# Optimization experiments

Hardware: AMD Instinct MI355X
Metric: run time of the kernel (lower is better)

## Reference

```python
import jax, jax.numpy as jnp
import numpy as np

DIM = 512
NUM_HEADS = 8
HEAD_SIZE = 64
INNER = NUM_HEADS * HEAD_SIZE  # 512


def setup_inputs() -> dict:
    key = jax.random.key(0)
    k1, k2, k3, k4, k5 = jax.random.split(key, 5)
    x = jax.random.normal(k1, (2, 4096, DIM), dtype=jnp.float32)
    # Linear params stored as [in, out] for y = x @ W + b (same math as torch Linear)
    w_qkv = jax.random.normal(k2, (DIM, INNER * 3), dtype=jnp.float32) * (1.0 / np.sqrt(DIM))
    b_qkv = jax.random.normal(k3, (INNER * 3,), dtype=jnp.float32) * 0.01
    w_out = jax.random.normal(k4, (INNER, DIM), dtype=jnp.float32) * (1.0 / np.sqrt(INNER))
    b_out = jax.random.normal(k5, (DIM,), dtype=jnp.float32) * 0.01
    return {"x": x, "w_qkv": w_qkv, "b_qkv": b_qkv, "w_out": w_out, "b_out": b_out}


def reference(x, w_qkv, b_qkv, w_out, b_out):
    b, n, _ = x.shape
    qkv = x @ w_qkv + b_qkv                      # [b, n, 3*inner]
    q, k, v = jnp.split(qkv, 3, axis=-1)          # each [b, n, inner]

    def heads(t):  # 'b n (h d) -> b h n d'
        return t.reshape(b, n, NUM_HEADS, HEAD_SIZE).transpose(0, 2, 1, 3)

    q, k, v = heads(q), heads(k), heads(v)
    scores = jnp.einsum('bhnd,bhmd->bhnm', q, k) / jnp.sqrt(jnp.float32(HEAD_SIZE))
    probs = jax.nn.softmax(scores, axis=-1)       # dropout is identity in eval
    out = jnp.einsum('bhnm,bhmd->bhnd', probs, v)
    out = out.transpose(0, 2, 1, 3).reshape(b, n, INNER)  # 'b h n d -> b n (h d)'
    return out @ w_out + b_out
```

## Files before the change

### kernel.cpp

```cpp
#include <hip/hip_runtime.h>

typedef __bf16 bf16;
typedef __bf16 bf16x8 __attribute__((ext_vector_type(8)));
typedef float f32x4 __attribute__((ext_vector_type(4)));
typedef unsigned u32x4 __attribute__((ext_vector_type(4)));
typedef unsigned u32;

#define MFMA16(a, b, c) __builtin_amdgcn_mfma_f32_16x16x32_bf16((a), (b), (c), 0, 0, 0)

static __device__ __forceinline__ bf16x8 ldg8(const bf16* p) {
  return *(const bf16x8*)p;
}
static __device__ __forceinline__ unsigned cvt_pk_bf16(float lo, float hi) {
  unsigned d;
  asm("v_cvt_pk_bf16_f32 %0, %1, %2" : "=v"(d) : "v"(lo), "v"(hi));
  return d;
}
static __device__ __forceinline__ void pl32_swap(unsigned& a, unsigned& b) {
  asm("v_permlane32_swap_b32 %0, %1" : "+v"(a), "+v"(b));
}
static __device__ __forceinline__ void pl16_swap(unsigned& a, unsigned& b) {
  asm("v_permlane16_swap_b32 %0, %1" : "+v"(a), "+v"(b));
}
static __device__ __forceinline__ void async_lds16(const bf16* g, bf16* l) {
  __builtin_amdgcn_global_load_lds(
      (const __attribute__((address_space(1))) u32*)(const void*)g,
      (__attribute__((address_space(3))) u32*)(void*)l, 16, 0, 0);
}


__global__ __launch_bounds__(256) void cvt_pack_x(const float* __restrict__ x,
                                                  bf16* __restrict__ Xp) {
  int mt = blockIdx.x, kc = blockIdx.y;
  int r = threadIdx.x >> 1;
  int khalf = threadIdx.x & 1;
  const float* src = x + (size_t)(mt * 128 + r) * 512 + kc * 32 + khalf * 16;
  float4 v0 = *(const float4*)(src + 0);
  float4 v1 = *(const float4*)(src + 4);
  float4 v2 = *(const float4*)(src + 8);
  float4 v3 = *(const float4*)(src + 12);
  bf16* tile = Xp + ((size_t)mt * 16 + kc) * 4096;
  bf16x8 a, b;
  a[0] = (bf16)v0.x; a[1] = (bf16)v0.y; a[2] = (bf16)v0.z; a[3] = (bf16)v0.w;
  a[4] = (bf16)v1.x; a[5] = (bf16)v1.y; a[6] = (bf16)v1.z; a[7] = (bf16)v1.w;
  b[0] = (bf16)v2.x; b[1] = (bf16)v2.y; b[2] = (bf16)v2.z; b[3] = (bf16)v2.w;
  b[4] = (bf16)v3.x; b[5] = (bf16)v3.y; b[6] = (bf16)v3.z; b[7] = (bf16)v3.w;
  int kc0 = khalf * 2;
  *(bf16x8*)&tile[(kc0 + 0) * 1024 + r * 8] = a;
  *(bf16x8*)&tile[(kc0 + 1) * 1024 + r * 8] = b;
}

__global__ __launch_bounds__(256) void transpose_pack_w(const float* __restrict__ W,
                                                        bf16* __restrict__ Wp,
                                                        int N) {
  __shared__ float tile[32 * 129];
  int kc = blockIdx.x, nt = blockIdx.y;
  int row = threadIdx.x >> 3;
  int c0 = (threadIdx.x & 7) * 16;
  const float* src = W + (size_t)(kc * 32 + row) * N + nt * 128 + c0;
#pragma unroll
  for (int i = 0; i < 4; i++) {
    float4 v = *(const float4*)(src + i * 4);
    tile[row * 129 + c0 + i * 4 + 0] = v.x;
    tile[row * 129 + c0 + i * 4 + 1] = v.y;
    tile[row * 129 + c0 + i * 4 + 2] = v.z;
    tile[row * 129 + c0 + i * 4 + 3] = v.w;
  }
  __syncthreads();
  bf16* dst = Wp + ((size_t)nt * 16 + kc) * 4096;
#pragma unroll
  for (int half = 0; half < 2; half++) {
    int U = threadIdx.x + half * 256;
    int kchunk = U >> 7, n = U & 127;
    bf16x8 o;
#pragma unroll
    for (int j = 0; j < 8; j++) o[j] = (bf16)tile[(kchunk * 8 + j) * 129 + n];
    *(bf16x8*)&dst[U * 8] = o;
  }
}

static __device__ __forceinline__ void stage_tile(const bf16* __restrict__ g,
                                                  bf16* l, int wave, int lane) {
#pragma unroll
  for (int c = 0; c < 2; c++) {
    int chunk = wave * 2 + c;
    async_lds16(g + chunk * 512 + lane * 8, l + chunk * 512);
  }
}

__device__ __forceinline__ void gemm128_core(const bf16* __restrict__ At,
                                             const bf16* __restrict__ Bt,
                                             bf16* Ab0, bf16* Ab1, bf16* Bb0,
                                             bf16* Bb1, int wave, int lane,
                                             int wr, int wc, int l16, int quad,
                                             f32x4 acc[4][4]) {
  stage_tile(At, Ab0, wave, lane);
  stage_tile(Bt, Bb0, wave, lane);
  __syncthreads();
#pragma unroll 2
  for (int kc = 0; kc < 16; kc++) {
    bf16* Ab = (kc & 1) ? Ab1 : Ab0;
    bf16* Bb = (kc & 1) ? Bb1 : Bb0;
    if (kc < 15) {
      bf16* An = (kc & 1) ? Ab0 : Ab1;
      bf16* Bn = (kc & 1) ? Bb0 : Bb1;
      stage_tile(At + (kc + 1) * 4096, An, wave, lane);
      stage_tile(Bt + (kc + 1) * 4096, Bn, wave, lane);
    }
    bf16x8 af[4], bf[4];
#pragma unroll
    for (int fi = 0; fi < 4; fi++)
      af[fi] = *(const bf16x8*)&Ab[(quad * 128 + wr * 64 + fi * 16 + l16) * 8];
#pragma unroll
    for (int fj = 0; fj < 4; fj++)
      bf[fj] = *(const bf16x8*)&Bb[(quad * 128 + wc * 64 + fj * 16 + l16) * 8];
    __builtin_amdgcn_s_setprio(1);
#pragma unroll
    for (int fi = 0; fi < 4; fi++)
#pragma unroll
      for (int fj = 0; fj < 4; fj++)
        acc[fi][fj] = MFMA16(af[fi], bf[fj], acc[fi][fj]);
    __builtin_amdgcn_s_setprio(0);
    __syncthreads();
  }
}

__global__ __launch_bounds__(256, 3) void qkv_gemm(const bf16* __restrict__ Xp,
                                                   const bf16* __restrict__ Wp1,
                                                   const float* __restrict__ bqkv,
                                                   bf16* __restrict__ Q,
                                                   bf16* __restrict__ Kh,
                                                   bf16* __restrict__ Vt) {
  int mt = blockIdx.x, nt = blockIdx.y;
  int tid = threadIdx.x;
  int wave = tid >> 6, lane = tid & 63;
  int l16 = lane & 15, quad = lane >> 4;
  int wr = wave >> 1, wc = wave & 1;

  __shared__ __align__(16) bf16 Ab[2][4096];
  __shared__ __align__(16) bf16 Bb[2][4096];

  f32x4 acc[4][4] = {};
  gemm128_core(Xp + (size_t)mt * 16 * 4096, Wp1 + (size_t)nt * 16 * 4096,
               Ab[0], Ab[1], Bb[0], Bb[1], wave, lane, wr, wc, l16, quad, acc);

#pragma unroll
  for (int fj = 0; fj < 4; fj++) {
    int c = nt * 128 + wc * 64 + fj * 16 + l16;
    float bias = bqkv[c];
    int which = c >> 9, inner = c & 511;
    int h = inner >> 6, d = inner & 63;
#pragma unroll
    for (int fi = 0; fi < 4; fi++) {
#pragma unroll
      for (int r = 0; r < 4; r++) {
        int m = mt * 128 + wr * 64 + fi * 16 + quad * 4 + r;
        int b = m >> 12, n = m & 4095;
        int bh = b * 8 + h;
        float v = acc[fi][fj][r] + bias;
        if (which == 0)
          Q[((size_t)bh * 4096 + n) * 64 + d] = (bf16)(v * 0.18033688f);
        else if (which == 1)
          Kh[((size_t)bh * 4096 + n) * 64 + d] = (bf16)v;
        else
          Vt[(((size_t)bh * 64 + (n >> 6)) * 64 + d) * 64 + (n & 63)] = (bf16)v;
      }
    }
  }
}

__global__ __launch_bounds__(256, 4) void flash_partial(const bf16* __restrict__ Q,
                                                        const bf16* __restrict__ K,
                                                        const bf16* __restrict__ Vt,
                                                        bf16* __restrict__ Opart,
                                                        float* __restrict__ Lpart) {
  int strip = blockIdx.x, bh = blockIdx.y, qtr = blockIdx.z;
  int tid = threadIdx.x;
  int wave = tid >> 6, lane = tid & 63;
  int l16 = lane & 15, quad = lane >> 4;

  const bf16* Qh = Q + (size_t)bh * 4096 * 64;
  const bf16* Kg = K + ((size_t)bh * 4096 + qtr * 1024) * 64;
  const bf16* Vg = Vt + (size_t)bh * 64 * 4096 + (size_t)qtr * 1024 * 64;

  __shared__ __align__(16) bf16 Klds[2][4096];
  __shared__ __align__(16) bf16 Vlds[2][4096];

  int qbase = strip * 128 + wave * 32;
  bf16x8 aq[2][2];
#pragma unroll
  for (int mt = 0; mt < 2; mt++) {
    const bf16* qr = Qh + (size_t)(qbase + mt * 16 + l16) * 64;
    aq[mt][0] = ldg8(qr + quad * 8);
    aq[mt][1] = ldg8(qr + 32 + quad * 8);
  }

  bf16x8 ones;
#pragma unroll
  for (int i = 0; i < 8; i++) ones[i] = (bf16)1.0f;

  f32x4 o[2][4] = {};
  f32x4 acc_l[2] = {};

  int e0 = tid * 8, e1 = (256 + tid) * 8;
  int r0 = e0 >> 6, r1 = e1 >> 6;
  int u0 = r0 * 8 + (((e0 & 63) >> 3) ^ (r0 & 7));
  int u1 = r1 * 8 + (((e1 & 63) >> 3) ^ (r1 & 7));

  bf16x8 kp0 = ldg8(Kg + e0), kp1 = ldg8(Kg + e1);
  bf16x8 vp0 = ldg8(Vg + e0), vp1 = ldg8(Vg + e1);

#pragma unroll 2
  for (int t = 0; t < 16; t++) {
    int cur = t & 1;
    bf16* kl = Klds[cur];
    bf16* vl = Vlds[cur];
    *(bf16x8*)&kl[u0 * 8] = kp0;
    *(bf16x8*)&kl[u1 * 8] = kp1;
    *(bf16x8*)&vl[u0 * 8] = vp0;
    *(bf16x8*)&vl[u1 * 8] = vp1;
    __syncthreads();

    if (t < 15) {
      const bf16* kg = Kg + (size_t)(t + 1) * 4096;
      const bf16* vg = Vg + (size_t)(t + 1) * 4096;
      kp0 = ldg8(kg + e0);
      kp1 = ldg8(kg + e1);
      vp0 = ldg8(vg + e0);
      vp1 = ldg8(vg + e1);
    }

#pragma unroll
    for (int h2 = 0; h2 < 2; h2++) {
      f32x4 s[2][2] = {};
      __builtin_amdgcn_s_setprio(1);
#pragma unroll
      for (int c2 = 0; c2 < 2; c2++) {
        int n = h2 * 32 + c2 * 16 + l16;
        bf16x8 k0 = *(const bf16x8*)&kl[(n * 8 + (quad ^ (n & 7))) * 8];
        bf16x8 k1 = *(const bf16x8*)&kl[(n * 8 + ((4 + quad) ^ (n & 7))) * 8];
#pragma unroll
        for (int mt = 0; mt < 2; mt++) {
          s[mt][c2] = MFMA16(k0, aq[mt][0], s[mt][c2]);
          s[mt][c2] = MFMA16(k1, aq[mt][1], s[mt][c2]);
        }
      }
      __builtin_amdgcn_s_setprio(0);

      bf16x8 pa[2];
#pragma unroll
      for (int mt = 0; mt < 2; mt++) {
        unsigned ue[2], wo[2];
#pragma unroll
        for (int c2 = 0; c2 < 2; c2++) {
          float p0 = __builtin_amdgcn_exp2f(s[mt][c2][0]);
          float p1 = __builtin_amdgcn_exp2f(s[mt][c2][1]);
          float p2 = __builtin_amdgcn_exp2f(s[mt][c2][2]);
          float p3 = __builtin_amdgcn_exp2f(s[mt][c2][3]);
          ue[c2] = cvt_pk_bf16(p0, p1);
          wo[c2] = cvt_pk_bf16(p2, p3);
        }
        pl32_swap(ue[0], ue[1]);
        pl16_swap(ue[0], ue[1]);
        pl32_swap(wo[0], wo[1]);
        pl16_swap(wo[0], wo[1]);
        u32x4 pk = {ue[0], wo[0], ue[1], wo[1]};
        pa[mt] = __builtin_bit_cast(bf16x8, pk);
      }

      __builtin_amdgcn_s_setprio(1);
      acc_l[0] = MFMA16(pa[0], ones, acc_l[0]);
      acc_l[1] = MFMA16(pa[1], ones, acc_l[1]);
#pragma unroll
      for (int ct = 0; ct < 4; ct++) {
        int d = ct * 16 + l16;
        bf16x8 bv = *(const bf16x8*)&vl[(d * 8 + ((h2 * 4 + quad) ^ (d & 7))) * 8];
        o[0][ct] = MFMA16(pa[0], bv, o[0][ct]);
        o[1][ct] = MFMA16(pa[1], bv, o[1][ct]);
      }
      __builtin_amdgcn_s_setprio(0);
    }
  }

  size_t ub = ((size_t)qtr * 16 + bh) * 32 + strip;
  bf16* op = Opart + ub * 8192;
#pragma unroll
  for (int mt = 0; mt < 2; mt++) {
#pragma unroll
    for (int ct = 0; ct < 4; ct++)
#pragma unroll
      for (int r = 0; r < 4; r++)
        op[(wave * 32 + mt * 16 + quad * 4 + r) * 64 + ct * 16 + l16] =
            (bf16)o[mt][ct][r];
    if (l16 == 0) {
#pragma unroll
      for (int r = 0; r < 4; r++)
        Lpart[ub * 128 + wave * 32 + mt * 16 + quad * 4 + r] = acc_l[mt][r];
    }
  }
}

__global__ __launch_bounds__(256) void flash_combine(const bf16* __restrict__ Opart,
                                                     const float* __restrict__ Lpart,
                                                     bf16* __restrict__ Ap) {
  int mt = blockIdx.x, kc = blockIdx.y;
  int b = mt >> 5, strip = mt & 31;
  int h = kc >> 1, d0 = (kc & 1) * 32;
  int bh = b * 8 + h;
  size_t u[4];
#pragma unroll
  for (int q = 0; q < 4; q++) u[q] = ((size_t)q * 16 + bh) * 32 + strip;
  bf16* dst = Ap + ((size_t)mt * 16 + kc) * 4096;
#pragma unroll
  for (int hf = 0; hf < 2; hf++) {
    int U = threadIdx.x + hf * 256;
    int kchunk = U >> 7, r = U & 127;
    float acc[8] = {};
    float ls = 0.f;
#pragma unroll
    for (int q = 0; q < 4; q++) {
      bf16x8 ov = ldg8(&Opart[u[q] * 8192 + r * 64 + d0 + kchunk * 8]);
#pragma unroll
      for (int j = 0; j < 8; j++) acc[j] += (float)ov[j];
      ls += Lpart[u[q] * 128 + r];
    }
    float rl = 1.0f / ls;
    bf16x8 o;
#pragma unroll
    for (int j = 0; j < 8; j++) o[j] = (bf16)(acc[j] * rl);
    *(bf16x8*)&dst[U * 8] = o;
  }
}

__global__ __launch_bounds__(256, 3) void out_gemm(const bf16* __restrict__ Ap,
                                                   const bf16* __restrict__ Wp2,
                                                   const float* __restrict__ bout,
                                                   float* __restrict__ Out) {
  int mt = blockIdx.x, nt = blockIdx.y;
  int tid = threadIdx.x;
  int wave = tid >> 6, lane = tid & 63;
  int l16 = lane & 15, quad = lane >> 4;
  int wr = wave >> 1, wc = wave & 1;

  __shared__ __align__(16) bf16 Ab[2][4096];
  __shared__ __align__(16) bf16 Bb[2][4096];

  f32x4 acc[4][4] = {};
  gemm128_core(Ap + (size_t)mt * 16 * 4096, Wp2 + (size_t)nt * 16 * 4096,
               Ab[0], Ab[1], Bb[0], Bb[1], wave, lane, wr, wc, l16, quad, acc);

#pragma unroll
  for (int fj = 0; fj < 4; fj++) {
    int c = nt * 128 + wc * 64 + fj * 16 + l16;
    float bias = bout[c];
#pragma unroll
    for (int fi = 0; fi < 4; fi++) {
#pragma unroll
      for (int r = 0; r < 4; r++) {
        int m = mt * 128 + wr * 64 + fi * 16 + quad * 4 + r;
        Out[(size_t)m * 512 + c] = acc[fi][fj][r] + bias;
      }
    }
  }
}

extern "C" void kernel_launch(void* const* d_in, const int* in_sizes, int n_in,
                              void* d_out, int out_size, void* d_ws,
                              size_t ws_size, hipStream_t stream) {
  const float* x = (const float*)d_in[0];
  const float* w_qkv = (const float*)d_in[1];
  const float* b_qkv = (const float*)d_in[2];
  const float* w_out = (const float*)d_in[3];
  const float* b_out = (const float*)d_in[4];
  float* out = (float*)d_out;

  char* ws = (char*)d_ws;
  bf16* Q = (bf16*)(ws + 0);
  bf16* K = (bf16*)(ws + 8388608);
  bf16* Vt = (bf16*)(ws + 16777216);
  bf16* Wp2 = (bf16*)(ws + 25165824);
  bf16* Opart = (bf16*)(ws + 25690112);
  float* Lpart = (float*)(ws + 59244544);
  bf16* Xp = (bf16*)(ws + 25690112);
  bf16* Wp1 = (bf16*)(ws + 34078720);
  bf16* Ap = (bf16*)(ws + 0);

  cvt_pack_x<<<dim3(64, 16), 256, 0, stream>>>(x, Xp);
  transpose_pack_w<<<dim3(16, 12), 256, 0, stream>>>(w_qkv, Wp1, 1536);
  transpose_pack_w<<<dim3(16, 4), 256, 0, stream>>>(w_out, Wp2, 512);
  qkv_gemm<<<dim3(64, 12), 256, 0, stream>>>(Xp, Wp1, b_qkv, Q, K, Vt);
  flash_partial<<<dim3(32, 16, 4), 256, 0, stream>>>(Q, K, Vt, Opart, Lpart);
  flash_combine<<<dim3(64, 16), 256, 0, stream>>>(Opart, Lpart, Ap);
  out_gemm<<<dim3(64, 4), 256, 0, stream>>>(Ap, Wp2, b_out, out);
}
```

Measured before the change: 208.2 us.

## Fuse x fp32-to-bf16 conversion into QKV GEMM and stage epilogue through LDS

Removes the separate cvt_pack_x kernel by having qkv_gemm load fp32 x directly, convert to bf16 in registers and write it into LDS. The two weight-pack launches are merged into one. The QKV epilogue now goes through an LDS tile so that Q, K and V^T are written with coalesced 16-byte stores instead of scattered 2-byte stores. Both GEMMs replace async global-to-LDS loads with register prefetch plus LDS stores. Each GEMM tile now re-reads fp32 x, twice the bytes of bf16, and the register-staged loads may hide latency less well than the async path.

```diff
diff --git a/kernel.cpp b/kernel.cpp
--- a/kernel.cpp
+++ b/kernel.cpp
@@ -4,7 +4,6 @@
 typedef __bf16 bf16x8 __attribute__((ext_vector_type(8)));
 typedef float f32x4 __attribute__((ext_vector_type(4)));
 typedef unsigned u32x4 __attribute__((ext_vector_type(4)));
-typedef unsigned u32;
 
 #define MFMA16(a, b, c) __builtin_amdgcn_mfma_f32_16x16x32_bf16((a), (b), (c), 0, 0, 0)
 
@@ -22,42 +21,27 @@
 static __device__ __forceinline__ void pl16_swap(unsigned& a, unsigned& b) {
   asm("v_permlane16_swap_b32 %0, %1" : "+v"(a), "+v"(b));
 }
-static __device__ __forceinline__ void async_lds16(const bf16* g, bf16* l) {
-  __builtin_amdgcn_global_load_lds(
-      (const __attribute__((address_space(1))) u32*)(const void*)g,
-      (__attribute__((address_space(3))) u32*)(void*)l, 16, 0, 0);
-}
-
-
-__global__ __launch_bounds__(256) void cvt_pack_x(const float* __restrict__ x,
-                                                  bf16* __restrict__ Xp) {
-  int mt = blockIdx.x, kc = blockIdx.y;
-  int r = threadIdx.x >> 1;
-  int khalf = threadIdx.x & 1;
-  const float* src = x + (size_t)(mt * 128 + r) * 512 + kc * 32 + khalf * 16;
-  float4 v0 = *(const float4*)(src + 0);
-  float4 v1 = *(const float4*)(src + 4);
-  float4 v2 = *(const float4*)(src + 8);
-  float4 v3 = *(const float4*)(src + 12);
-  bf16* tile = Xp + ((size_t)mt * 16 + kc) * 4096;
-  bf16x8 a, b;
-  a[0] = (bf16)v0.x; a[1] = (bf16)v0.y; a[2] = (bf16)v0.z; a[3] = (bf16)v0.w;
-  a[4] = (bf16)v1.x; a[5] = (bf16)v1.y; a[6] = (bf16)v1.z; a[7] = (bf16)v1.w;
-  b[0] = (bf16)v2.x; b[1] = (bf16)v2.y; b[2] = (bf16)v2.z; b[3] = (bf16)v2.w;
-  b[4] = (bf16)v3.x; b[5] = (bf16)v3.y; b[6] = (bf16)v3.z; b[7] = (bf16)v3.w;
-  int kc0 = khalf * 2;
-  *(bf16x8*)&tile[(kc0 + 0) * 1024 + r * 8] = a;
-  *(bf16x8*)&tile[(kc0 + 1) * 1024 + r * 8] = b;
-}
-
-__global__ __launch_bounds__(256) void transpose_pack_w(const float* __restrict__ W,
-                                                        bf16* __restrict__ Wp,
-                                                        int N) {
+
+
+__global__ __launch_bounds__(256) void pack_weights(const float* __restrict__ Wqkv,
+                                                    const float* __restrict__ Wout,
+                                                    bf16* __restrict__ Wp1,
+                                                    bf16* __restrict__ Wp2) {
   __shared__ float tile[32 * 129];
   int kc = blockIdx.x, nt = blockIdx.y;
+  const float* W;
+  bf16* dst;
+  int N, ntl;
+  if (nt < 12) {
+    W = Wqkv; N = 1536; ntl = nt;
+    dst = Wp1 + ((size_t)ntl * 16 + kc) * 4096;
+  } else {
+    W = Wout; N = 512; ntl = nt - 12;
+    dst = Wp2 + ((size_t)ntl * 16 + kc) * 4096;
+  }
   int row = threadIdx.x >> 3;
   int c0 = (threadIdx.x & 7) * 16;
-  const float* src = W + (size_t)(kc * 32 + row) * N + nt * 128 + c0;
+  const float* src = W + (size_t)(kc * 32 + row) * N + ntl * 128 + c0;
 #pragma unroll
   for (int i = 0; i < 4; i++) {
     float4 v = *(const float4*)(src + i * 4);
@@ -67,7 +51,6 @@
     tile[row * 129 + c0 + i * 4 + 3] = v.w;
   }
   __syncthreads();
-  bf16* dst = Wp + ((size_t)nt * 16 + kc) * 4096;
 #pragma unroll
   for (int half = 0; half < 2; half++) {
     int U = threadIdx.x + half * 256;
@@ -79,53 +62,7 @@
   }
 }
 
-static __device__ __forceinline__ void stage_tile(const bf16* __restrict__ g,
-                                                  bf16* l, int wave, int lane) {
-#pragma unroll
-  for (int c = 0; c < 2; c++) {
-    int chunk = wave * 2 + c;
-    async_lds16(g + chunk * 512 + lane * 8, l + chunk * 512);
-  }
-}
-
-__device__ __forceinline__ void gemm128_core(const bf16* __restrict__ At,
-                                             const bf16* __restrict__ Bt,
-                                             bf16* Ab0, bf16* Ab1, bf16* Bb0,
-                                             bf16* Bb1, int wave, int lane,
-                                             int wr, int wc, int l16, int quad,
-                                             f32x4 acc[4][4]) {
-  stage_tile(At, Ab0, wave, lane);
-  stage_tile(Bt, Bb0, wave, lane);
-  __syncthreads();
-#pragma unroll 2
-  for (int kc = 0; kc < 16; kc++) {
-    bf16* Ab = (kc & 1) ? Ab1 : Ab0;
-    bf16* Bb = (kc & 1) ? Bb1 : Bb0;
-    if (kc < 15) {
-      bf16* An = (kc & 1) ? Ab0 : Ab1;
-      bf16* Bn = (kc & 1) ? Bb0 : Bb1;
-      stage_tile(At + (kc + 1) * 4096, An, wave, lane);
-      stage_tile(Bt + (kc + 1) * 4096, Bn, wave, lane);
-    }
-    bf16x8 af[4], bf[4];
-#pragma unroll
-    for (int fi = 0; fi < 4; fi++)
-      af[fi] = *(const bf16x8*)&Ab[(quad * 128 + wr * 64 + fi * 16 + l16) * 8];
-#pragma unroll
-    for (int fj = 0; fj < 4; fj++)
-      bf[fj] = *(const bf16x8*)&Bb[(quad * 128 + wc * 64 + fj * 16 + l16) * 8];
-    __builtin_amdgcn_s_setprio(1);
-#pragma unroll
-    for (int fi = 0; fi < 4; fi++)
-#pragma unroll
-      for (int fj = 0; fj < 4; fj++)
-        acc[fi][fj] = MFMA16(af[fi], bf[fj], acc[fi][fj]);
-    __builtin_amdgcn_s_setprio(0);
-    __syncthreads();
-  }
-}
-
-__global__ __launch_bounds__(256, 3) void qkv_gemm(const bf16* __restrict__ Xp,
+__global__ __launch_bounds__(256, 3) void qkv_gemm(const float* __restrict__ x,
                                                    const bf16* __restrict__ Wp1,
                                                    const float* __restrict__ bqkv,
                                                    bf16* __restrict__ Q,
@@ -137,34 +74,127 @@
   int l16 = lane & 15, quad = lane >> 4;
   int wr = wave >> 1, wc = wave & 1;
 
-  __shared__ __align__(16) bf16 Ab[2][4096];
-  __shared__ __align__(16) bf16 Bb[2][4096];
+  __shared__ __align__(16) bf16 SM[16384];
+
+  int r = tid >> 1, khalf = tid & 1;
+  const float* xs = x + (size_t)(mt * 128 + r) * 512 + khalf * 16;
+  const bf16* Bt = Wp1 + (size_t)nt * 16 * 4096;
+  int lwA0 = ((khalf * 2 + 0) * 128 + r) * 8;
+  int lwA1 = ((khalf * 2 + 1) * 128 + r) * 8;
+
+  float4 fa0 = *(const float4*)(xs + 0);
+  float4 fa1 = *(const float4*)(xs + 4);
+  float4 fa2 = *(const float4*)(xs + 8);
+  float4 fa3 = *(const float4*)(xs + 12);
+  bf16x8 pb0 = ldg8(Bt + tid * 8), pb1 = ldg8(Bt + 2048 + tid * 8);
 
   f32x4 acc[4][4] = {};
-  gemm128_core(Xp + (size_t)mt * 16 * 4096, Wp1 + (size_t)nt * 16 * 4096,
-               Ab[0], Ab[1], Bb[0], Bb[1], wave, lane, wr, wc, l16, quad, acc);
-
-#pragma unroll
-  for (int fj = 0; fj < 4; fj++) {
-    int c = nt * 128 + wc * 64 + fj * 16 + l16;
-    float bias = bqkv[c];
-    int which = c >> 9, inner = c & 511;
-    int h = inner >> 6, d = inner & 63;
-#pragma unroll
-    for (int fi = 0; fi < 4; fi++) {
-#pragma unroll
-      for (int r = 0; r < 4; r++) {
-        int m = mt * 128 + wr * 64 + fi * 16 + quad * 4 + r;
-        int b = m >> 12, n = m & 4095;
+#pragma unroll 2
+  for (int kc = 0; kc < 16; kc++) {
+    bf16* A = SM + (kc & 1) * 4096;
+    bf16* B = SM + 8192 + (kc & 1) * 4096;
+    bf16x8 a0, a1;
+    a0[0] = (bf16)fa0.x; a0[1] = (bf16)fa0.y; a0[2] = (bf16)fa0.z; a0[3] = (bf16)fa0.w;
+    a0[4] = (bf16)fa1.x; a0[5] = (bf16)fa1.y; a0[6] = (bf16)fa1.z; a0[7] = (bf16)fa1.w;
+    a1[0] = (bf16)fa2.x; a1[1] = (bf16)fa2.y; a1[2] = (bf16)fa2.z; a1[3] = (bf16)fa2.w;
+    a1[4] = (bf16)fa3.x; a1[5] = (bf16)fa3.y; a1[6] = (bf16)fa3.z; a1[7] = (bf16)fa3.w;
+    *(bf16x8*)&A[lwA0] = a0;
+    *(bf16x8*)&A[lwA1] = a1;
+    *(bf16x8*)&B[tid * 8] = pb0;
+    *(bf16x8*)&B[2048 + tid * 8] = pb1;
+    __syncthreads();
+    if (kc < 15) {
+      const float* xn = xs + (kc + 1) * 32;
+      fa0 = *(const float4*)(xn + 0);
+      fa1 = *(const float4*)(xn + 4);
+      fa2 = *(const float4*)(xn + 8);
+      fa3 = *(const float4*)(xn + 12);
+      const bf16* bn = Bt + (kc + 1) * 4096;
+      pb0 = ldg8(bn + tid * 8);
+      pb1 = ldg8(bn + 2048 + tid * 8);
+    }
+    bf16x8 af[4], bfr[4];
+#pragma unroll
+    for (int fi = 0; fi < 4; fi++)
+      af[fi] = *(const bf16x8*)&A[(quad * 128 + wr * 64 + fi * 16 + l16) * 8];
+#pragma unroll
+    for (int fj = 0; fj < 4; fj++)
+      bfr[fj] = *(const bf16x8*)&B[(quad * 128 + wc * 64 + fj * 16 + l16) * 8];
+    __builtin_amdgcn_s_setprio(1);
+#pragma unroll
+    for (int fi = 0; fi < 4; fi++)
+#pragma unroll
+      for (int fj = 0; fj < 4; fj++)
+        acc[fi][fj] = MFMA16(af[fi], bfr[fj], acc[fi][fj]);
+    __builtin_amdgcn_s_setprio(0);
+  }
+
+  __syncthreads();
+  const int TS = 72;
+  int b = mt >> 5;
+
+  if (nt < 8) {
+    bool isQ = nt < 4;
+    bf16* dstb = isQ ? Q : Kh;
+    int hb = isQ ? nt * 2 : (nt - 4) * 2;
+#pragma unroll
+    for (int ph = 0; ph < 2; ph++) {
+      if (wc == ph) {
+#pragma unroll
+        for (int fj = 0; fj < 4; fj++) {
+          float bias = bqkv[nt * 128 + wc * 64 + fj * 16 + l16];
+#pragma unroll
+          for (int fi = 0; fi < 4; fi++)
+#pragma unroll
+            for (int rr = 0; rr < 4; rr++) {
+              float v = acc[fi][fj][rr] + bias;
+              if (isQ) v *= 0.18033688f;
+              SM[(wr * 64 + fi * 16 + quad * 4 + rr) * TS + fj * 16 + l16] =
+                  (bf16)v;
+            }
+        }
+      }
+      __syncthreads();
+      int bh = b * 8 + hb + ph;
+      bf16* dh = dstb + (size_t)bh * 4096 * 64 + (size_t)((mt & 31) * 128) * 64;
+#pragma unroll
+      for (int i = 0; i < 4; i++) {
+        int U = tid + i * 256;
+        int mr = U >> 3, oct = U & 7;
+        bf16x8 v = ldg8(&SM[mr * TS + oct * 8]);
+        *(bf16x8*)&dh[(size_t)mr * 64 + oct * 8] = v;
+      }
+      __syncthreads();
+    }
+  } else {
+    int h0 = (nt - 8) * 2;
+#pragma unroll
+    for (int ph = 0; ph < 2; ph++) {
+      if (wr == ph) {
+#pragma unroll
+        for (int fj = 0; fj < 4; fj++) {
+          float bias = bqkv[nt * 128 + wc * 64 + fj * 16 + l16];
+          int cp = wc * 64 + fj * 16 + l16;
+#pragma unroll
+          for (int fi = 0; fi < 4; fi++)
+#pragma unroll
+            for (int rr = 0; rr < 4; rr++)
+              SM[cp * TS + fi * 16 + quad * 4 + rr] =
+                  (bf16)(acc[fi][fj][rr] + bias);
+        }
+      }
+      __syncthreads();
+      int nb = (mt & 31) * 2 + ph;
+#pragma unroll
+      for (int i = 0; i < 4; i++) {
+        int U = tid + i * 256;
+        int cp = U >> 3, oct = U & 7;
+        int h = h0 + (cp >> 6), d = cp & 63;
         int bh = b * 8 + h;
-        float v = acc[fi][fj][r] + bias;
-        if (which == 0)
-          Q[((size_t)bh * 4096 + n) * 64 + d] = (bf16)(v * 0.18033688f);
-        else if (which == 1)
-          Kh[((size_t)bh * 4096 + n) * 64 + d] = (bf16)v;
-        else
-          Vt[(((size_t)bh * 64 + (n >> 6)) * 64 + d) * 64 + (n & 63)] = (bf16)v;
-      }
+        bf16x8 v = ldg8(&SM[cp * TS + oct * 8]);
+        *(bf16x8*)&Vt[(((size_t)bh * 64 + nb) * 64 + d) * 64 + oct * 8] = v;
+      }
+      __syncthreads();
     }
   }
 }
@@ -342,12 +372,46 @@
   int l16 = lane & 15, quad = lane >> 4;
   int wr = wave >> 1, wc = wave & 1;
 
-  __shared__ __align__(16) bf16 Ab[2][4096];
-  __shared__ __align__(16) bf16 Bb[2][4096];
+  __shared__ __align__(16) bf16 SM[16384];
+
+  const bf16* At = Ap + (size_t)mt * 16 * 4096;
+  const bf16* Bt = Wp2 + (size_t)nt * 16 * 4096;
+  bf16x8 pa0 = ldg8(At + tid * 8), pa1 = ldg8(At + 2048 + tid * 8);
+  bf16x8 pb0 = ldg8(Bt + tid * 8), pb1 = ldg8(Bt + 2048 + tid * 8);
 
   f32x4 acc[4][4] = {};
-  gemm128_core(Ap + (size_t)mt * 16 * 4096, Wp2 + (size_t)nt * 16 * 4096,
-               Ab[0], Ab[1], Bb[0], Bb[1], wave, lane, wr, wc, l16, quad, acc);
+#pragma unroll 2
+  for (int kc = 0; kc < 16; kc++) {
+    bf16* A = SM + (kc & 1) * 4096;
+    bf16* B = SM + 8192 + (kc & 1) * 4096;
+    *(bf16x8*)&A[tid * 8] = pa0;
+    *(bf16x8*)&A[2048 + tid * 8] = pa1;
+    *(bf16x8*)&B[tid * 8] = pb0;
+    *(bf16x8*)&B[2048 + tid * 8] = pb1;
+    __syncthreads();
+    if (kc < 15) {
+      const bf16* an = At + (kc + 1) * 4096;
+      const bf16* bn = Bt + (kc + 1) * 4096;
+      pa0 = ldg8(an + tid * 8);
+      pa1 = ldg8(an + 2048 + tid * 8);
+      pb0 = ldg8(bn + tid * 8);
+      pb1 = ldg8(bn + 2048 + tid * 8);
+    }
+    bf16x8 af[4], bfr[4];
+#pragma unroll
+    for (int fi = 0; fi < 4; fi++)
+      af[fi] = *(const bf16x8*)&A[(quad * 128 + wr * 64 + fi * 16 + l16) * 8];
+#pragma unroll
+    for (int fj = 0; fj < 4; fj++)
+      bfr[fj] = *(const bf16x8*)&B[(quad * 128 + wc * 64 + fj * 16 + l16) * 8];
+    __builtin_amdgcn_s_setprio(1);
+#pragma unroll
+    for (int fi = 0; fi < 4; fi++)
+#pragma unroll
+      for (int fj = 0; fj < 4; fj++)
+        acc[fi][fj] = MFMA16(af[fi], bfr[fj], acc[fi][fj]);
+    __builtin_amdgcn_s_setprio(0);
+  }
 
 #pragma unroll
   for (int fj = 0; fj < 4; fj++) {
@@ -381,14 +445,11 @@
   bf16* Wp2 = (bf16*)(ws + 25165824);
   bf16* Opart = (bf16*)(ws + 25690112);
   float* Lpart = (float*)(ws + 59244544);
-  bf16* Xp = (bf16*)(ws + 25690112);
   bf16* Wp1 = (bf16*)(ws + 34078720);
   bf16* Ap = (bf16*)(ws + 0);
 
-  cvt_pack_x<<<dim3(64, 16), 256, 0, stream>>>(x, Xp);
-  transpose_pack_w<<<dim3(16, 12), 256, 0, stream>>>(w_qkv, Wp1, 1536);
-  transpose_pack_w<<<dim3(16, 4), 256, 0, stream>>>(w_out, Wp2, 512);
-  qkv_gemm<<<dim3(64, 12), 256, 0, stream>>>(Xp, Wp1, b_qkv, Q, K, Vt);
+  pack_weights<<<dim3(16, 16), 256, 0, stream>>>(w_qkv, w_out, Wp1, Wp2);
+  qkv_gemm<<<dim3(64, 12), 256, 0, stream>>>(x, Wp1, b_qkv, Q, K, Vt);
   flash_partial<<<dim3(32, 16, 4), 256, 0, stream>>>(Q, K, Vt, Opart, Lpart);
   flash_combine<<<dim3(64, 16), 256, 0, stream>>>(Opart, Lpart, Ap);
   out_gemm<<<dim3(64, 4), 256, 0, stream>>>(Ap, Wp2, b_out, out);
```

Result: faster. 197.6 us (-5.1%).
